# Performance work log

Hardware: AMD Instinct MI355X
Metric: run time of the kernel (lower is better)

## Reference

```python
import jax, jax.numpy as jnp
import numpy as np

N_NODES = 50000


def _gcn_conv(h, src, dst, W, b, n_nodes):
    """PyG GCNConv: add self-loops, symmetric deg^{-1/2} normalization,
    linear transform, scatter-add aggregation at target nodes."""
    h = h @ W  # [N, out]
    # self-loops
    loop = jnp.arange(n_nodes, dtype=src.dtype)
    s = jnp.concatenate([src, loop])  # source j
    d = jnp.concatenate([dst, loop])  # target i
    ones = jnp.ones(s.shape[0], dtype=h.dtype)
    deg = jax.ops.segment_sum(ones, d, num_segments=n_nodes)  # in-degree incl. self-loop
    dinv = jnp.where(deg > 0, jax.lax.rsqrt(deg), 0.0)
    norm = dinv[s] * dinv[d]  # [E+N]
    msg = h[s] * norm[:, None]  # gather + scale, [E+N, out]
    out = jax.ops.segment_sum(msg, d, num_segments=n_nodes)  # scatter-add
    return out + b


def reference(x, edge_index, q_emb, W1, b1, W2, b2, Wq, bq):
    src, dst = edge_index[0], edge_index[1]
    n = x.shape[0]
    # dropout rates are 0.0 -> identity
    h1 = jax.nn.relu(_gcn_conv(x, src, dst, W1, b1, n))
    h2 = _gcn_conv(h1, src, dst, W2, b2, n)
    ques = q_emb @ Wq + bq
    return (ques, h2)


def setup_inputs() -> dict:
    key = jax.random.key(0)
    ks = jax.random.split(key, 9)
    d = 128
    sc = 1.0 / np.sqrt(d)
    return {
        "x": jax.random.normal(ks[0], (N_NODES, d), dtype=jnp.float32),
        "edge_index": jax.random.randint(ks[1], (2, 800000), 0, N_NODES, dtype=jnp.int64),
        "q_emb": jax.random.normal(ks[2], (20000, d), dtype=jnp.float32),
        "W1": jax.random.normal(ks[3], (d, d), dtype=jnp.float32) * sc,
        "b1": jax.random.normal(ks[4], (d,), dtype=jnp.float32) * 0.01,
        "W2": jax.random.normal(ks[5], (d, d), dtype=jnp.float32) * sc,
        "b2": jax.random.normal(ks[6], (d,), dtype=jnp.float32) * 0.01,
        "Wq": jax.random.normal(ks[7], (d, d), dtype=jnp.float32) * sc,
        "bq": jax.random.normal(ks[8], (d,), dtype=jnp.float32) * 0.01,
    }
```

## Files before the change

### kernel.cpp

```cpp
#include <hip/hip_runtime.h>

#define D 128
#define NFB 256
#define CAP 64

typedef __attribute__((ext_vector_type(8))) short bf16x8;
typedef __attribute__((ext_vector_type(4))) float f32x4;

__device__ __forceinline__ unsigned short f2b(float v) {
    unsigned u = __float_as_uint(v);
    unsigned r = u + 0x7fffu + ((u >> 16) & 1u);
    return (unsigned short)(r >> 16);
}
__device__ __forceinline__ float b2f(unsigned short h) {
    return __uint_as_float(((unsigned)h) << 16);
}


__device__ __forceinline__ void gemm_body(const float* Af,
                                          const float* __restrict__ W,
                                          const float* bias, unsigned short* Cb,
                                          float* Cf, int M, int bid, int outf,
                                          char* smem) {
    int lane = threadIdx.x & 63;
    int wave = threadIdx.x >> 6;
    int m16 = (bid * 4 + wave) * 16;
    if (m16 >= M) return;
    int mrow = lane & 15;
    int quad = lane >> 4;

    f32x4 acc[8];
#pragma unroll
    for (int nt = 0; nt < 8; ++nt) acc[nt] = (f32x4){0.f, 0.f, 0.f, 0.f};

    int arow = m16 + mrow;

#pragma unroll
    for (int ks = 0; ks < 4; ++ks) {
        bf16x8 ah, al;
        const float* ap = Af + (size_t)arow * D + ks * 32 + quad * 8;
        float4 v0 = *(const float4*)ap;
        float4 v1 = *(const float4*)(ap + 4);
        float vv[8] = {v0.x, v0.y, v0.z, v0.w, v1.x, v1.y, v1.z, v1.w};
#pragma unroll
        for (int j = 0; j < 8; ++j) {
            unsigned short h = f2b(vv[j]);
            ah[j] = (short)h;
            al[j] = (short)f2b(vv[j] - b2f(h));
        }
#pragma unroll
        for (int nt = 0; nt < 8; ++nt) {
            const float* wp = W + (size_t)(ks * 32 + quad * 8) * D + nt * 16 + mrow;
            bf16x8 wf;
#pragma unroll
            for (int j = 0; j < 8; ++j) wf[j] = (short)f2b(wp[j * D]);
            acc[nt] = __builtin_amdgcn_mfma_f32_16x16x32_bf16(ah, wf, acc[nt], 0, 0, 0);
            acc[nt] = __builtin_amdgcn_mfma_f32_16x16x32_bf16(al, wf, acc[nt], 0, 0, 0);
        }
    }

    if (outf == 0) {
        unsigned short* myl = (unsigned short*)smem + wave * 16 * 136;
#pragma unroll
        for (int nt = 0; nt < 8; ++nt) {
            int col = nt * 16 + mrow;
#pragma unroll
            for (int r = 0; r < 4; ++r)
                myl[(quad * 4 + r) * 136 + col] = f2b(acc[nt][r]);
        }
#pragma unroll
        for (int R = 0; R < 16; ++R) {
            unsigned int v = *(const unsigned int*)&myl[R * 136 + lane * 2];
            ((unsigned int*)(Cb + (size_t)(m16 + R) * D))[lane] = v;
        }
    } else {
#pragma unroll
        for (int nt = 0; nt < 8; ++nt) {
            int col = nt * 16 + mrow;
            float bv = bias[col];
#pragma unroll
            for (int r = 0; r < 4; ++r)
                Cf[(size_t)(m16 + quad * 4 + r) * D + col] = acc[nt][r] + bv;
        }
    }
}

__global__ __launch_bounds__(256) void frontfill(const float* __restrict__ x,
                                                 const float* __restrict__ q,
                                                 const float* __restrict__ W1,
                                                 const float* __restrict__ Wq,
                                                 const float* __restrict__ bq,
                                                 unsigned short* __restrict__ Cb,
                                                 float* __restrict__ outq,
                                                 const int* __restrict__ src,
                                                 const int* __restrict__ dst,
                                                 int* __restrict__ cnt,
                                                 int* __restrict__ colv,
                                                 int N, int MQ, int E, int nbN) {
    __shared__ char smem[4 * 16 * 136 * 2];
    int b = blockIdx.x;
    if (b < NFB) {
        const int4* d4 = (const int4*)dst;
        const int4* s4 = (const int4*)src;
        int n4 = E >> 2;
        int stride = NFB * 256;
        for (int idx = b * 256 + threadIdx.x; idx < n4; idx += stride) {
            int4 dv = d4[idx];
            int4 sv = s4[idx];
            int slot;
            slot = atomicAdd(&cnt[dv.x], 1);
            if (slot < CAP) colv[(size_t)dv.x * CAP + slot] = sv.x;
            slot = atomicAdd(&cnt[dv.y], 1);
            if (slot < CAP) colv[(size_t)dv.y * CAP + slot] = sv.y;
            slot = atomicAdd(&cnt[dv.z], 1);
            if (slot < CAP) colv[(size_t)dv.z * CAP + slot] = sv.z;
            slot = atomicAdd(&cnt[dv.w], 1);
            if (slot < CAP) colv[(size_t)dv.w * CAP + slot] = sv.w;
        }
        for (int e = (n4 << 2) + b * 256 + threadIdx.x; e < E; e += stride) {
            int d = dst[e];
            int slot = atomicAdd(&cnt[d], 1);
            if (slot < CAP) colv[(size_t)d * CAP + slot] = src[e];
        }
        return;
    }
    b -= NFB;
    if (b < nbN)
        gemm_body(x, W1, nullptr, Cb, nullptr, N, b, 0, smem);
    else
        gemm_body(q, Wq, bq, nullptr, outq, MQ, b - nbN, 1, smem);
}

__device__ __forceinline__ void agg_node(const bf16x8* __restrict__ T8,
                                         const int* __restrict__ colv,
                                         const int* __restrict__ cnt,
                                         int i, int ci, int lane, int g, int l16,
                                         float acc[8]) {
#pragma unroll
    for (int k = 0; k < 8; ++k) acc[k] = 0.f;
    int jv = 0;
    float wv = 0.f;
    if (lane < ci) {
        jv = colv[i * CAP + lane];
        wv = rsqrtf((float)(cnt[jv] + 1));
    }
    int t = 0;
    for (; t + 16 <= ci; t += 16) {
        int j0 = __shfl(jv, t + g);
        int j1 = __shfl(jv, t + 4 + g);
        int j2 = __shfl(jv, t + 8 + g);
        int j3 = __shfl(jv, t + 12 + g);
        float w0 = __shfl(wv, t + g);
        float w1 = __shfl(wv, t + 4 + g);
        float w2 = __shfl(wv, t + 8 + g);
        float w3 = __shfl(wv, t + 12 + g);
        bf16x8 r0 = T8[(size_t)j0 * 16 + l16];
        bf16x8 r1 = T8[(size_t)j1 * 16 + l16];
        bf16x8 r2 = T8[(size_t)j2 * 16 + l16];
        bf16x8 r3 = T8[(size_t)j3 * 16 + l16];
#pragma unroll
        for (int k = 0; k < 8; ++k) acc[k] = fmaf(w0, b2f((unsigned short)r0[k]), acc[k]);
#pragma unroll
        for (int k = 0; k < 8; ++k) acc[k] = fmaf(w1, b2f((unsigned short)r1[k]), acc[k]);
#pragma unroll
        for (int k = 0; k < 8; ++k) acc[k] = fmaf(w2, b2f((unsigned short)r2[k]), acc[k]);
#pragma unroll
        for (int k = 0; k < 8; ++k) acc[k] = fmaf(w3, b2f((unsigned short)r3[k]), acc[k]);
    }
    for (; t < ci; t += 4) {
        int j = __shfl(jv, t + g);
        float w = __shfl(wv, t + g);
        if (w > 0.f) {
            bf16x8 r = T8[(size_t)j * 16 + l16];
#pragma unroll
            for (int k = 0; k < 8; ++k) acc[k] = fmaf(w, b2f((unsigned short)r[k]), acc[k]);
        }
    }
#pragma unroll
    for (int k = 0; k < 8; ++k) {
        acc[k] += __shfl_xor(acc[k], 16);
        acc[k] += __shfl_xor(acc[k], 32);
    }
}

__global__ __launch_bounds__(512) void agg1_gemm(const unsigned short* __restrict__ Tb,
                                                 const int* __restrict__ colv,
                                                 const int* __restrict__ cnt,
                                                 const float* __restrict__ bias,
                                                 const float* __restrict__ W2,
                                                 unsigned short* __restrict__ Cb2,
                                                 int N) {
    __shared__ unsigned short AH[16 * 136];
    __shared__ unsigned short AL[16 * 136];
    int wave = threadIdx.x >> 6;
    int lane = threadIdx.x & 63;
    int g = lane >> 4;
    int l16 = lane & 15;
    int node0 = blockIdx.x * 16;
    const bf16x8* T8 = (const bf16x8*)Tb;

#pragma unroll
    for (int sub = 0; sub < 2; ++sub) {
        int row = wave * 2 + sub;
        int i = node0 + row;
        float acc[8];
        if (i < N) {
            int deg = cnt[i];
            int ci = (deg < CAP) ? deg : CAP;
            agg_node(T8, colv, cnt, i, ci, lane, g, l16, acc);
            if (g == 0) {
                float di = rsqrtf((float)(deg + 1));
                bf16x8 selfr = T8[(size_t)i * 16 + l16];
                float4 b0 = ((const float4*)bias)[l16 * 2];
                float4 b1v = ((const float4*)bias)[l16 * 2 + 1];
                float bb[8] = {b0.x, b0.y, b0.z, b0.w, b1v.x, b1v.y, b1v.z, b1v.w};
                bf16x8 h, l;
#pragma unroll
                for (int k = 0; k < 8; ++k) {
                    float r = di * acc[k] + di * di * b2f((unsigned short)selfr[k]) + bb[k];
                    r = fmaxf(r, 0.f);
                    unsigned short hh = f2b(r);
                    h[k] = (short)hh;
                    l[k] = (short)f2b(r - b2f(hh));
                }
                *(bf16x8*)&AH[row * 136 + l16 * 8] = h;
                *(bf16x8*)&AL[row * 136 + l16 * 8] = l;
            }
        } else if (g == 0) {
            bf16x8 z = (bf16x8){0, 0, 0, 0, 0, 0, 0, 0};
            *(bf16x8*)&AH[row * 136 + l16 * 8] = z;
            *(bf16x8*)&AL[row * 136 + l16 * 8] = z;
        }
    }
    __syncthreads();

    int nt = wave;
    int mrow = l16;
    int quad = g;
    f32x4 acc2 = (f32x4){0.f, 0.f, 0.f, 0.f};
#pragma unroll
    for (int ks = 0; ks < 4; ++ks) {
        bf16x8 ah = *(const bf16x8*)&AH[mrow * 136 + ks * 32 + quad * 8];
        bf16x8 al = *(const bf16x8*)&AL[mrow * 136 + ks * 32 + quad * 8];
        const float* wp = W2 + (size_t)(ks * 32 + quad * 8) * D + nt * 16 + mrow;
        bf16x8 wf;
#pragma unroll
        for (int j = 0; j < 8; ++j) wf[j] = (short)f2b(wp[j * D]);
        acc2 = __builtin_amdgcn_mfma_f32_16x16x32_bf16(ah, wf, acc2, 0, 0, 0);
        acc2 = __builtin_amdgcn_mfma_f32_16x16x32_bf16(al, wf, acc2, 0, 0, 0);
    }
    __syncthreads();
    {
        int col = nt * 16 + mrow;
#pragma unroll
        for (int r = 0; r < 4; ++r) {
            int gi = node0 + quad * 4 + r;
            float dr = (gi < N) ? rsqrtf((float)(cnt[gi] + 1)) : 0.f;
            AH[(quad * 4 + r) * 136 + col] = f2b(acc2[r] * dr);
        }
    }
    __syncthreads();
#pragma unroll
    for (int k = 0; k < 2; ++k) {
        int idx = threadIdx.x + k * 512;
        int row = idx >> 6;
        int c = idx & 63;
        if (node0 + row < N) {
            unsigned int v = *(const unsigned int*)&AH[row * 136 + c * 2];
            ((unsigned int*)(Cb2 + (size_t)(node0 + row) * D))[c] = v;
        }
    }
}

__global__ __launch_bounds__(512) void aggregate2(const unsigned short* __restrict__ Tb,
                                                  const int* __restrict__ colv,
                                                  const int* __restrict__ cnt,
                                                  const float* __restrict__ bias,
                                                  float* __restrict__ Of, int N) {
    int wave = threadIdx.x >> 6;
    int lane = threadIdx.x & 63;
    int i = blockIdx.x * 8 + wave;
    if (i >= N) return;
    int g = lane >> 4;
    int l16 = lane & 15;
    const bf16x8* T8 = (const bf16x8*)Tb;

    int deg = cnt[i];
    int ci = (deg < CAP) ? deg : CAP;
    bf16x8 selfr = T8[(size_t)i * 16 + l16];
    float4 b0 = ((const float4*)bias)[l16 * 2];
    float4 b1v = ((const float4*)bias)[l16 * 2 + 1];

    float acc[8];
#pragma unroll
    for (int k = 0; k < 8; ++k) acc[k] = 0.f;

    int jv = (lane < ci) ? colv[i * CAP + lane] : 0;
    int t = 0;
    for (; t + 16 <= ci; t += 16) {
        int j0 = __shfl(jv, t + g);
        int j1 = __shfl(jv, t + 4 + g);
        int j2 = __shfl(jv, t + 8 + g);
        int j3 = __shfl(jv, t + 12 + g);
        bf16x8 r0 = T8[(size_t)j0 * 16 + l16];
        bf16x8 r1 = T8[(size_t)j1 * 16 + l16];
        bf16x8 r2 = T8[(size_t)j2 * 16 + l16];
        bf16x8 r3 = T8[(size_t)j3 * 16 + l16];
#pragma unroll
        for (int k = 0; k < 8; ++k)
            acc[k] += b2f((unsigned short)r0[k]) + b2f((unsigned short)r1[k]) +
                      b2f((unsigned short)r2[k]) + b2f((unsigned short)r3[k]);
    }
    for (; t < ci; t += 4) {
        int j = __shfl(jv, t + g);
        if (t + g < ci) {
            bf16x8 r = T8[(size_t)j * 16 + l16];
#pragma unroll
            for (int k = 0; k < 8; ++k) acc[k] += b2f((unsigned short)r[k]);
        }
    }

#pragma unroll
    for (int k = 0; k < 8; ++k) {
        acc[k] += __shfl_xor(acc[k], 16);
        acc[k] += __shfl_xor(acc[k], 32);
    }

    if (g == 0) {
        float di = rsqrtf((float)(deg + 1));
        float bb[8] = {b0.x, b0.y, b0.z, b0.w, b1v.x, b1v.y, b1v.z, b1v.w};
        float4 r0, r1;
        r0.x = di * (acc[0] + b2f((unsigned short)selfr[0])) + bb[0];
        r0.y = di * (acc[1] + b2f((unsigned short)selfr[1])) + bb[1];
        r0.z = di * (acc[2] + b2f((unsigned short)selfr[2])) + bb[2];
        r0.w = di * (acc[3] + b2f((unsigned short)selfr[3])) + bb[3];
        r1.x = di * (acc[4] + b2f((unsigned short)selfr[4])) + bb[4];
        r1.y = di * (acc[5] + b2f((unsigned short)selfr[5])) + bb[5];
        r1.z = di * (acc[6] + b2f((unsigned short)selfr[6])) + bb[6];
        r1.w = di * (acc[7] + b2f((unsigned short)selfr[7])) + bb[7];
        ((float4*)Of)[(size_t)i * 32 + l16 * 2] = r0;
        ((float4*)Of)[(size_t)i * 32 + l16 * 2 + 1] = r1;
    }
}


static inline char* carve(char*& w, size_t bytes) {
    char* p = w;
    w += (bytes + 255) & ~(size_t)255;
    return p;
}

extern "C" void kernel_launch(void* const* d_in, const int* in_sizes, int n_in,
                              void* d_out, int out_size, void* d_ws, size_t ws_size,
                              hipStream_t stream) {
    const float* x  = (const float*)d_in[0];
    const int*   ei = (const int*)d_in[1];
    const float* q  = (const float*)d_in[2];
    const float* W1 = (const float*)d_in[3];
    const float* b1 = (const float*)d_in[4];
    const float* W2 = (const float*)d_in[5];
    const float* b2 = (const float*)d_in[6];
    const float* Wq = (const float*)d_in[7];
    const float* bq = (const float*)d_in[8];

    int N  = in_sizes[0] / D;
    int E  = in_sizes[1] / 2;
    int MQ = in_sizes[2] / D;

    const int* srcv = ei;
    const int* dstv = ei + E;

    char* w = (char*)d_ws;
    unsigned short* Cb   = (unsigned short*)carve(w, (size_t)N * D * 2);
    unsigned short* Cb2  = (unsigned short*)carve(w, (size_t)N * D * 2);
    int*            colv = (int*)carve(w, (size_t)N * CAP * 4);
    int*            cnt  = (int*)carve(w, (size_t)N * 4);

    float* outq = (float*)d_out;
    float* outh = outq + (size_t)MQ * D;

    int nbN = (N + 63) / 64;
    int nbQ = (MQ + 63) / 64;

    hipMemsetAsync(cnt, 0, (size_t)N * 4, stream);
    frontfill<<<NFB + nbN + nbQ, 256, 0, stream>>>(x, q, W1, Wq, bq, Cb, outq,
                                                   srcv, dstv, cnt, colv,
                                                   N, MQ, E, nbN);
    agg1_gemm<<<(N + 15) / 16, 512, 0, stream>>>(Cb, colv, cnt, b1, W2, Cb2, N);
    aggregate2<<<(N + 7) / 8, 512, 0, stream>>>(Cb2, colv, cnt, b2, outh, N);
}
```

Baseline: 227.4 us.

## Fuse all stages into one persistent cooperative kernel with grid syncs

Replaces the memset plus three kernel launches with a single cooperative persistent kernel that zeroes counts, builds adjacency and runs the GEMMs, then does both aggregations, separated by grid-wide syncs. Each block covers multiple virtual tiles in grid-stride loops. The aim is to remove launch gaps and kernel-boundary drain/tail costs. It adds grid-sync overhead, can lower occupancy because shared memory is larger and registers are shared across phases, and falls back to the old path if the cooperative launch fails.

```diff
diff --git a/kernel.cpp b/kernel.cpp
--- a/kernel.cpp
+++ b/kernel.cpp
@@ -1,4 +1,7 @@
 #include <hip/hip_runtime.h>
+#include <hip/hip_cooperative_groups.h>
+
+namespace cg = cooperative_groups;
 
 #define D 128
 #define NFB 256
@@ -17,13 +20,42 @@
 }
 
 
-__device__ __forceinline__ void gemm_body(const float* Af,
+__device__ __forceinline__ void fill_vb(int vb, int ltid,
+                                        const int* __restrict__ src,
+                                        const int* __restrict__ dst,
+                                        int* __restrict__ cnt,
+                                        int* __restrict__ colv, int E) {
+    const int4* d4 = (const int4*)dst;
+    const int4* s4 = (const int4*)src;
+    int n4 = E >> 2;
+    int stride = NFB * 256;
+    for (int idx = vb * 256 + ltid; idx < n4; idx += stride) {
+        int4 dv = d4[idx];
+        int4 sv = s4[idx];
+        int slot;
+        slot = atomicAdd(&cnt[dv.x], 1);
+        if (slot < CAP) colv[(size_t)dv.x * CAP + slot] = sv.x;
+        slot = atomicAdd(&cnt[dv.y], 1);
+        if (slot < CAP) colv[(size_t)dv.y * CAP + slot] = sv.y;
+        slot = atomicAdd(&cnt[dv.z], 1);
+        if (slot < CAP) colv[(size_t)dv.z * CAP + slot] = sv.z;
+        slot = atomicAdd(&cnt[dv.w], 1);
+        if (slot < CAP) colv[(size_t)dv.w * CAP + slot] = sv.w;
+    }
+    for (int e = (n4 << 2) + vb * 256 + ltid; e < E; e += stride) {
+        int d = dst[e];
+        int slot = atomicAdd(&cnt[d], 1);
+        if (slot < CAP) colv[(size_t)d * CAP + slot] = src[e];
+    }
+}
+
+__device__ __forceinline__ void gemm_tile(const float* Af,
                                           const float* __restrict__ W,
                                           const float* bias, unsigned short* Cb,
                                           float* Cf, int M, int bid, int outf,
-                                          char* smem) {
-    int lane = threadIdx.x & 63;
-    int wave = threadIdx.x >> 6;
+                                          char* smem, int ltid) {
+    int lane = ltid & 63;
+    int wave = ltid >> 6;
     int m16 = (bid * 4 + wave) * 16;
     if (m16 >= M) return;
     int mrow = lane & 15;
@@ -84,6 +116,279 @@
         }
     }
 }
+
+__device__ __forceinline__ void agg_node(const bf16x8* __restrict__ T8,
+                                         const int* __restrict__ colv,
+                                         const int* __restrict__ cnt,
+                                         int i, int ci, int lane, int g, int l16,
+                                         float acc[8]) {
+#pragma unroll
+    for (int k = 0; k < 8; ++k) acc[k] = 0.f;
+    int jv = 0;
+    float wv = 0.f;
+    if (lane < ci) {
+        jv = colv[i * CAP + lane];
+        wv = rsqrtf((float)(cnt[jv] + 1));
+    }
+    int t = 0;
+    for (; t + 16 <= ci; t += 16) {
+        int j0 = __shfl(jv, t + g);
+        int j1 = __shfl(jv, t + 4 + g);
+        int j2 = __shfl(jv, t + 8 + g);
+        int j3 = __shfl(jv, t + 12 + g);
+        float w0 = __shfl(wv, t + g);
+        float w1 = __shfl(wv, t + 4 + g);
+        float w2 = __shfl(wv, t + 8 + g);
+        float w3 = __shfl(wv, t + 12 + g);
+        bf16x8 r0 = T8[(size_t)j0 * 16 + l16];
+        bf16x8 r1 = T8[(size_t)j1 * 16 + l16];
+        bf16x8 r2 = T8[(size_t)j2 * 16 + l16];
+        bf16x8 r3 = T8[(size_t)j3 * 16 + l16];
+#pragma unroll
+        for (int k = 0; k < 8; ++k) acc[k] = fmaf(w0, b2f((unsigned short)r0[k]), acc[k]);
+#pragma unroll
+        for (int k = 0; k < 8; ++k) acc[k] = fmaf(w1, b2f((unsigned short)r1[k]), acc[k]);
+#pragma unroll
+        for (int k = 0; k < 8; ++k) acc[k] = fmaf(w2, b2f((unsigned short)r2[k]), acc[k]);
+#pragma unroll
+        for (int k = 0; k < 8; ++k) acc[k] = fmaf(w3, b2f((unsigned short)r3[k]), acc[k]);
+    }
+    for (; t < ci; t += 4) {
+        int j = __shfl(jv, t + g);
+        float w = __shfl(wv, t + g);
+        if (w > 0.f) {
+            bf16x8 r = T8[(size_t)j * 16 + l16];
+#pragma unroll
+            for (int k = 0; k < 8; ++k) acc[k] = fmaf(w, b2f((unsigned short)r[k]), acc[k]);
+        }
+    }
+#pragma unroll
+    for (int k = 0; k < 8; ++k) {
+        acc[k] += __shfl_xor(acc[k], 16);
+        acc[k] += __shfl_xor(acc[k], 32);
+    }
+}
+
+__device__ __forceinline__ void agg1_body(int grp, unsigned short* AH,
+                                          unsigned short* AL,
+                                          const unsigned short* __restrict__ Tb,
+                                          const int* __restrict__ colv,
+                                          const int* __restrict__ cnt,
+                                          const float* __restrict__ bias,
+                                          const float* __restrict__ W2,
+                                          unsigned short* __restrict__ Cb2, int N) {
+    __syncthreads();
+    int wave = threadIdx.x >> 6;
+    int lane = threadIdx.x & 63;
+    int g = lane >> 4;
+    int l16 = lane & 15;
+    int node0 = grp * 16;
+    const bf16x8* T8 = (const bf16x8*)Tb;
+
+#pragma unroll
+    for (int sub = 0; sub < 2; ++sub) {
+        int row = wave * 2 + sub;
+        int i = node0 + row;
+        float acc[8];
+        if (i < N) {
+            int deg = cnt[i];
+            int ci = (deg < CAP) ? deg : CAP;
+            agg_node(T8, colv, cnt, i, ci, lane, g, l16, acc);
+            if (g == 0) {
+                float di = rsqrtf((float)(deg + 1));
+                bf16x8 selfr = T8[(size_t)i * 16 + l16];
+                float4 b0 = ((const float4*)bias)[l16 * 2];
+                float4 b1v = ((const float4*)bias)[l16 * 2 + 1];
+                float bb[8] = {b0.x, b0.y, b0.z, b0.w, b1v.x, b1v.y, b1v.z, b1v.w};
+                bf16x8 h, l;
+#pragma unroll
+                for (int k = 0; k < 8; ++k) {
+                    float r = di * acc[k] + di * di * b2f((unsigned short)selfr[k]) + bb[k];
+                    r = fmaxf(r, 0.f);
+                    unsigned short hh = f2b(r);
+                    h[k] = (short)hh;
+                    l[k] = (short)f2b(r - b2f(hh));
+                }
+                *(bf16x8*)&AH[row * 136 + l16 * 8] = h;
+                *(bf16x8*)&AL[row * 136 + l16 * 8] = l;
+            }
+        } else if (g == 0) {
+            bf16x8 z = (bf16x8){0, 0, 0, 0, 0, 0, 0, 0};
+            *(bf16x8*)&AH[row * 136 + l16 * 8] = z;
+            *(bf16x8*)&AL[row * 136 + l16 * 8] = z;
+        }
+    }
+    __syncthreads();
+
+    int nt = wave;
+    int mrow = l16;
+    int quad = g;
+    f32x4 acc2 = (f32x4){0.f, 0.f, 0.f, 0.f};
+#pragma unroll
+    for (int ks = 0; ks < 4; ++ks) {
+        bf16x8 ah = *(const bf16x8*)&AH[mrow * 136 + ks * 32 + quad * 8];
+        bf16x8 al = *(const bf16x8*)&AL[mrow * 136 + ks * 32 + quad * 8];
+        const float* wp = W2 + (size_t)(ks * 32 + quad * 8) * D + nt * 16 + mrow;
+        bf16x8 wf;
+#pragma unroll
+        for (int j = 0; j < 8; ++j) wf[j] = (short)f2b(wp[j * D]);
+        acc2 = __builtin_amdgcn_mfma_f32_16x16x32_bf16(ah, wf, acc2, 0, 0, 0);
+        acc2 = __builtin_amdgcn_mfma_f32_16x16x32_bf16(al, wf, acc2, 0, 0, 0);
+    }
+    __syncthreads();
+    {
+        int col = nt * 16 + mrow;
+#pragma unroll
+        for (int r = 0; r < 4; ++r) {
+            int gi = node0 + quad * 4 + r;
+            float dr = (gi < N) ? rsqrtf((float)(cnt[gi] + 1)) : 0.f;
+            AH[(quad * 4 + r) * 136 + col] = f2b(acc2[r] * dr);
+        }
+    }
+    __syncthreads();
+#pragma unroll
+    for (int k = 0; k < 2; ++k) {
+        int idx = threadIdx.x + k * 512;
+        int row = idx >> 6;
+        int c = idx & 63;
+        if (node0 + row < N) {
+            unsigned int v = *(const unsigned int*)&AH[row * 136 + c * 2];
+            ((unsigned int*)(Cb2 + (size_t)(node0 + row) * D))[c] = v;
+        }
+    }
+}
+
+__device__ __forceinline__ void agg2_body(int grp,
+                                          const unsigned short* __restrict__ Tb,
+                                          const int* __restrict__ colv,
+                                          const int* __restrict__ cnt,
+                                          const float* __restrict__ bias,
+                                          float* __restrict__ Of, int N) {
+    int wave = threadIdx.x >> 6;
+    int lane = threadIdx.x & 63;
+    int i = grp * 8 + wave;
+    if (i >= N) return;
+    int g = lane >> 4;
+    int l16 = lane & 15;
+    const bf16x8* T8 = (const bf16x8*)Tb;
+
+    int deg = cnt[i];
+    int ci = (deg < CAP) ? deg : CAP;
+    bf16x8 selfr = T8[(size_t)i * 16 + l16];
+    float4 b0 = ((const float4*)bias)[l16 * 2];
+    float4 b1v = ((const float4*)bias)[l16 * 2 + 1];
+
+    float acc[8];
+#pragma unroll
+    for (int k = 0; k < 8; ++k) acc[k] = 0.f;
+
+    int jv = (lane < ci) ? colv[i * CAP + lane] : 0;
+    int t = 0;
+    for (; t + 16 <= ci; t += 16) {
+        int j0 = __shfl(jv, t + g);
+        int j1 = __shfl(jv, t + 4 + g);
+        int j2 = __shfl(jv, t + 8 + g);
+        int j3 = __shfl(jv, t + 12 + g);
+        bf16x8 r0 = T8[(size_t)j0 * 16 + l16];
+        bf16x8 r1 = T8[(size_t)j1 * 16 + l16];
+        bf16x8 r2 = T8[(size_t)j2 * 16 + l16];
+        bf16x8 r3 = T8[(size_t)j3 * 16 + l16];
+#pragma unroll
+        for (int k = 0; k < 8; ++k)
+            acc[k] += b2f((unsigned short)r0[k]) + b2f((unsigned short)r1[k]) +
+                      b2f((unsigned short)r2[k]) + b2f((unsigned short)r3[k]);
+    }
+    for (; t < ci; t += 4) {
+        int j = __shfl(jv, t + g);
+        if (t + g < ci) {
+            bf16x8 r = T8[(size_t)j * 16 + l16];
+#pragma unroll
+            for (int k = 0; k < 8; ++k) acc[k] += b2f((unsigned short)r[k]);
+        }
+    }
+
+#pragma unroll
+    for (int k = 0; k < 8; ++k) {
+        acc[k] += __shfl_xor(acc[k], 16);
+        acc[k] += __shfl_xor(acc[k], 32);
+    }
+
+    if (g == 0) {
+        float di = rsqrtf((float)(deg + 1));
+        float bb[8] = {b0.x, b0.y, b0.z, b0.w, b1v.x, b1v.y, b1v.z, b1v.w};
+        float4 r0, r1;
+        r0.x = di * (acc[0] + b2f((unsigned short)selfr[0])) + bb[0];
+        r0.y = di * (acc[1] + b2f((unsigned short)selfr[1])) + bb[1];
+        r0.z = di * (acc[2] + b2f((unsigned short)selfr[2])) + bb[2];
+        r0.w = di * (acc[3] + b2f((unsigned short)selfr[3])) + bb[3];
+        r1.x = di * (acc[4] + b2f((unsigned short)selfr[4])) + bb[4];
+        r1.y = di * (acc[5] + b2f((unsigned short)selfr[5])) + bb[5];
+        r1.z = di * (acc[6] + b2f((unsigned short)selfr[6])) + bb[6];
+        r1.w = di * (acc[7] + b2f((unsigned short)selfr[7])) + bb[7];
+        ((float4*)Of)[(size_t)i * 32 + l16 * 2] = r0;
+        ((float4*)Of)[(size_t)i * 32 + l16 * 2 + 1] = r1;
+    }
+}
+
+
+__global__ __launch_bounds__(512) void mega(const float* x, const float* q,
+                                            const float* W1, const float* Wq,
+                                            const float* bq, const float* W2,
+                                            const float* b1, const float* b2,
+                                            unsigned short* Cb, unsigned short* Cb2,
+                                            float* outq, float* outh,
+                                            const int* src, const int* dst,
+                                            int* cnt, int* colv,
+                                            int N, int MQ, int E, int nbN, int nbQ) {
+    __shared__ char smem[2 * 4 * 16 * 136 * 2];
+    cg::grid_group grid = cg::this_grid();
+    int G = gridDim.x;
+
+    {
+        int n4 = N >> 2;
+        for (int idx = blockIdx.x * 512 + threadIdx.x; idx < n4; idx += G * 512)
+            ((int4*)cnt)[idx] = make_int4(0, 0, 0, 0);
+        for (int k = (n4 << 2) + blockIdx.x * 512 + threadIdx.x; k < N; k += G * 512)
+            cnt[k] = 0;
+    }
+    grid.sync();
+
+    {
+        int half = threadIdx.x >> 8;
+        int ltid = threadIdx.x & 255;
+        int nvb = NFB + nbN + nbQ;
+        for (int vb = blockIdx.x * 2 + half; vb < nvb; vb += G * 2) {
+            if (vb < NFB) {
+                fill_vb(vb, ltid, src, dst, cnt, colv, E);
+            } else {
+                int b = vb - NFB;
+                if (b < nbN)
+                    gemm_tile(x, W1, nullptr, Cb, nullptr, N, b, 0,
+                              smem + half * 17408, ltid);
+                else
+                    gemm_tile(q, Wq, bq, nullptr, outq, MQ, b - nbN, 1,
+                              smem + half * 17408, ltid);
+            }
+        }
+    }
+    grid.sync();
+
+    {
+        unsigned short* AH = (unsigned short*)smem;
+        unsigned short* AL = (unsigned short*)(smem + 4352);
+        int ngrp = (N + 15) / 16;
+        for (int grp = blockIdx.x; grp < ngrp; grp += G)
+            agg1_body(grp, AH, AL, Cb, colv, cnt, b1, W2, Cb2, N);
+    }
+    grid.sync();
+
+    {
+        int ngrp = (N + 7) / 8;
+        for (int grp = blockIdx.x; grp < ngrp; grp += G)
+            agg2_body(grp, Cb2, colv, cnt, b2, outh, N);
+    }
+}
+
 
 __global__ __launch_bounds__(256) void frontfill(const float* __restrict__ x,
                                                  const float* __restrict__ q,
@@ -100,87 +405,14 @@
     __shared__ char smem[4 * 16 * 136 * 2];
     int b = blockIdx.x;
     if (b < NFB) {
-        const int4* d4 = (const int4*)dst;
-        const int4* s4 = (const int4*)src;
-        int n4 = E >> 2;
-        int stride = NFB * 256;
-        for (int idx = b * 256 + threadIdx.x; idx < n4; idx += stride) {
-            int4 dv = d4[idx];
-            int4 sv = s4[idx];
-            int slot;
-            slot = atomicAdd(&cnt[dv.x], 1);
-            if (slot < CAP) colv[(size_t)dv.x * CAP + slot] = sv.x;
-            slot = atomicAdd(&cnt[dv.y], 1);
-            if (slot < CAP) colv[(size_t)dv.y * CAP + slot] = sv.y;
-            slot = atomicAdd(&cnt[dv.z], 1);
-            if (slot < CAP) colv[(size_t)dv.z * CAP + slot] = sv.z;
-            slot = atomicAdd(&cnt[dv.w], 1);
-            if (slot < CAP) colv[(size_t)dv.w * CAP + slot] = sv.w;
-        }
-        for (int e = (n4 << 2) + b * 256 + threadIdx.x; e < E; e += stride) {
-            int d = dst[e];
-            int slot = atomicAdd(&cnt[d], 1);
-            if (slot < CAP) colv[(size_t)d * CAP + slot] = src[e];
-        }
+        fill_vb(b, threadIdx.x, src, dst, cnt, colv, E);
         return;
     }
     b -= NFB;
     if (b < nbN)
-        gemm_body(x, W1, nullptr, Cb, nullptr, N, b, 0, smem);
+        gemm_tile(x, W1, nullptr, Cb, nullptr, N, b, 0, smem, threadIdx.x);
     else
-        gemm_body(q, Wq, bq, nullptr, outq, MQ, b - nbN, 1, smem);
-}
-
-__device__ __forceinline__ void agg_node(const bf16x8* __restrict__ T8,
-                                         const int* __restrict__ colv,
-                                         const int* __restrict__ cnt,
-                                         int i, int ci, int lane, int g, int l16,
-                                         float acc[8]) {
-#pragma unroll
-    for (int k = 0; k < 8; ++k) acc[k] = 0.f;
-    int jv = 0;
-    float wv = 0.f;
-    if (lane < ci) {
-        jv = colv[i * CAP + lane];
-        wv = rsqrtf((float)(cnt[jv] + 1));
-    }
-    int t = 0;
-    for (; t + 16 <= ci; t += 16) {
-        int j0 = __shfl(jv, t + g);
-        int j1 = __shfl(jv, t + 4 + g);
-        int j2 = __shfl(jv, t + 8 + g);
-        int j3 = __shfl(jv, t + 12 + g);
-        float w0 = __shfl(wv, t + g);
-        float w1 = __shfl(wv, t + 4 + g);
-        float w2 = __shfl(wv, t + 8 + g);
-        float w3 = __shfl(wv, t + 12 + g);
-        bf16x8 r0 = T8[(size_t)j0 * 16 + l16];
-        bf16x8 r1 = T8[(size_t)j1 * 16 + l16];
-        bf16x8 r2 = T8[(size_t)j2 * 16 + l16];
-        bf16x8 r3 = T8[(size_t)j3 * 16 + l16];
-#pragma unroll
-        for (int k = 0; k < 8; ++k) acc[k] = fmaf(w0, b2f((unsigned short)r0[k]), acc[k]);
-#pragma unroll
-        for (int k = 0; k < 8; ++k) acc[k] = fmaf(w1, b2f((unsigned short)r1[k]), acc[k]);
-#pragma unroll
-        for (int k = 0; k < 8; ++k) acc[k] = fmaf(w2, b2f((unsigned short)r2[k]), acc[k]);
-#pragma unroll
-        for (int k = 0; k < 8; ++k) acc[k] = fmaf(w3, b2f((unsigned short)r3[k]), acc[k]);
-    }
-    for (; t < ci; t += 4) {
-        int j = __shfl(jv, t + g);
-        float w = __shfl(wv, t + g);
-        if (w > 0.f) {
-            bf16x8 r = T8[(size_t)j * 16 + l16];
-#pragma unroll
-            for (int k = 0; k < 8; ++k) acc[k] = fmaf(w, b2f((unsigned short)r[k]), acc[k]);
-        }
-    }
-#pragma unroll
-    for (int k = 0; k < 8; ++k) {
-        acc[k] += __shfl_xor(acc[k], 16);
-        acc[k] += __shfl_xor(acc[k], 32);
-    }
+        gemm_tile(q, Wq, bq, nullptr, outq, MQ, b - nbN, 1, smem, threadIdx.x);
 }
 
 __global__ __launch_bounds__(512) void agg1_gemm(const unsigned short* __restrict__ Tb,
@@ -192,84 +424,7 @@
                                                  int N) {
     __shared__ unsigned short AH[16 * 136];
     __shared__ unsigned short AL[16 * 136];
-    int wave = threadIdx.x >> 6;
-    int lane = threadIdx.x & 63;
-    int g = lane >> 4;
-    int l16 = lane & 15;
-    int node0 = blockIdx.x * 16;
-    const bf16x8* T8 = (const bf16x8*)Tb;
-
-#pragma unroll
-    for (int sub = 0; sub < 2; ++sub) {
-        int row = wave * 2 + sub;
-        int i = node0 + row;
-        float acc[8];
-        if (i < N) {
-            int deg = cnt[i];
-            int ci = (deg < CAP) ? deg : CAP;
-            agg_node(T8, colv, cnt, i, ci, lane, g, l16, acc);
-            if (g == 0) {
-                float di = rsqrtf((float)(deg + 1));
-                bf16x8 selfr = T8[(size_t)i * 16 + l16];
-                float4 b0 = ((const float4*)bias)[l16 * 2];
-                float4 b1v = ((const float4*)bias)[l16 * 2 + 1];
-                float bb[8] = {b0.x, b0.y, b0.z, b0.w, b1v.x, b1v.y, b1v.z, b1v.w};
-                bf16x8 h, l;
-#pragma unroll
-                for (int k = 0; k < 8; ++k) {
-                    float r = di * acc[k] + di * di * b2f((unsigned short)selfr[k]) + bb[k];
-                    r = fmaxf(r, 0.f);
-                    unsigned short hh = f2b(r);
-                    h[k] = (short)hh;
-                    l[k] = (short)f2b(r - b2f(hh));
-                }
-                *(bf16x8*)&AH[row * 136 + l16 * 8] = h;
-                *(bf16x8*)&AL[row * 136 + l16 * 8] = l;
-            }
-        } else if (g == 0) {
-            bf16x8 z = (bf16x8){0, 0, 0, 0, 0, 0, 0, 0};
-            *(bf16x8*)&AH[row * 136 + l16 * 8] = z;
-            *(bf16x8*)&AL[row * 136 + l16 * 8] = z;
-        }
-    }
-    __syncthreads();
-
-    int nt = wave;
-    int mrow = l16;
-    int quad = g;
-    f32x4 acc2 = (f32x4){0.f, 0.f, 0.f, 0.f};
-#pragma unroll
-    for (int ks = 0; ks < 4; ++ks) {
-        bf16x8 ah = *(const bf16x8*)&AH[mrow * 136 + ks * 32 + quad * 8];
-        bf16x8 al = *(const bf16x8*)&AL[mrow * 136 + ks * 32 + quad * 8];
-        const float* wp = W2 + (size_t)(ks * 32 + quad * 8) * D + nt * 16 + mrow;
-        bf16x8 wf;
-#pragma unroll
-        for (int j = 0; j < 8; ++j) wf[j] = (short)f2b(wp[j * D]);
-        acc2 = __builtin_amdgcn_mfma_f32_16x16x32_bf16(ah, wf, acc2, 0, 0, 0);
-        acc2 = __builtin_amdgcn_mfma_f32_16x16x32_bf16(al, wf, acc2, 0, 0, 0);
-    }
-    __syncthreads();
-    {
-        int col = nt * 16 + mrow;
-#pragma unroll
-        for (int r = 0; r < 4; ++r) {
-            int gi = node0 + quad * 4 + r;
-            float dr = (gi < N) ? rsqrtf((float)(cnt[gi] + 1)) : 0.f;
-            AH[(quad * 4 + r) * 136 + col] = f2b(acc2[r] * dr);
-        }
-    }
-    __syncthreads();
-#pragma unroll
-    for (int k = 0; k < 2; ++k) {
-        int idx = threadIdx.x + k * 512;
-        int row = idx >> 6;
-        int c = idx & 63;
-        if (node0 + row < N) {
-            unsigned int v = *(const unsigned int*)&AH[row * 136 + c * 2];
-            ((unsigned int*)(Cb2 + (size_t)(node0 + row) * D))[c] = v;
-        }
-    }
+    agg1_body(blockIdx.x, AH, AL, Tb, colv, cnt, bias, W2, Cb2, N);
 }
 
 __global__ __launch_bounds__(512) void aggregate2(const unsigned short* __restrict__ Tb,
@@ -277,70 +432,7 @@
                                                   const int* __restrict__ cnt,
                                                   const float* __restrict__ bias,
                                                   float* __restrict__ Of, int N) {
-    int wave = threadIdx.x >> 6;
-    int lane = threadIdx.x & 63;
-    int i = blockIdx.x * 8 + wave;
-    if (i >= N) return;
-    int g = lane >> 4;
-    int l16 = lane & 15;
-    const bf16x8* T8 = (const bf16x8*)Tb;
-
-    int deg = cnt[i];
-    int ci = (deg < CAP) ? deg : CAP;
-    bf16x8 selfr = T8[(size_t)i * 16 + l16];
-    float4 b0 = ((const float4*)bias)[l16 * 2];
-    float4 b1v = ((const float4*)bias)[l16 * 2 + 1];
-
-    float acc[8];
-#pragma unroll
-    for (int k = 0; k < 8; ++k) acc[k] = 0.f;
-
-    int jv = (lane < ci) ? colv[i * CAP + lane] : 0;
-    int t = 0;
-    for (; t + 16 <= ci; t += 16) {
-        int j0 = __shfl(jv, t + g);
-        int j1 = __shfl(jv, t + 4 + g);
-        int j2 = __shfl(jv, t + 8 + g);
-        int j3 = __shfl(jv, t + 12 + g);
-        bf16x8 r0 = T8[(size_t)j0 * 16 + l16];
-        bf16x8 r1 = T8[(size_t)j1 * 16 + l16];
-        bf16x8 r2 = T8[(size_t)j2 * 16 + l16];
-        bf16x8 r3 = T8[(size_t)j3 * 16 + l16];
-#pragma unroll
-        for (int k = 0; k < 8; ++k)
-            acc[k] += b2f((unsigned short)r0[k]) + b2f((unsigned short)r1[k]) +
-                      b2f((unsigned short)r2[k]) + b2f((unsigned short)r3[k]);
-    }
-    for (; t < ci; t += 4) {
-        int j = __shfl(jv, t + g);
-        if (t + g < ci) {
-            bf16x8 r = T8[(size_t)j * 16 + l16];
-#pragma unroll
-            for (int k = 0; k < 8; ++k) acc[k] += b2f((unsigned short)r[k]);
-        }
-    }
-
-#pragma unroll
-    for (int k = 0; k < 8; ++k) {
-        acc[k] += __shfl_xor(acc[k], 16);
-        acc[k] += __shfl_xor(acc[k], 32);
-    }
-
-    if (g == 0) {
-        float di = rsqrtf((float)(deg + 1));
-        float bb[8] = {b0.x, b0.y, b0.z, b0.w, b1v.x, b1v.y, b1v.z, b1v.w};
-        float4 r0, r1;
-        r0.x = di * (acc[0] + b2f((unsigned short)selfr[0])) + bb[0];
-        r0.y = di * (acc[1] + b2f((unsigned short)selfr[1])) + bb[1];
-        r0.z = di * (acc[2] + b2f((unsigned short)selfr[2])) + bb[2];
-        r0.w = di * (acc[3] + b2f((unsigned short)selfr[3])) + bb[3];
-        r1.x = di * (acc[4] + b2f((unsigned short)selfr[4])) + bb[4];
-        r1.y = di * (acc[5] + b2f((unsigned short)selfr[5])) + bb[5];
-        r1.z = di * (acc[6] + b2f((unsigned short)selfr[6])) + bb[6];
-        r1.w = di * (acc[7] + b2f((unsigned short)selfr[7])) + bb[7];
-        ((float4*)Of)[(size_t)i * 32 + l16 * 2] = r0;
-        ((float4*)Of)[(size_t)i * 32 + l16 * 2 + 1] = r1;
-    }
+    agg2_body(blockIdx.x, Tb, colv, cnt, bias, Of, N);
 }
 
 
@@ -382,10 +474,45 @@
     int nbN = (N + 63) / 64;
     int nbQ = (MQ + 63) / 64;
 
-    hipMemsetAsync(cnt, 0, (size_t)N * 4, stream);
-    frontfill<<<NFB + nbN + nbQ, 256, 0, stream>>>(x, q, W1, Wq, bq, Cb, outq,
-                                                   srcv, dstv, cnt, colv,
-                                                   N, MQ, E, nbN);
-    agg1_gemm<<<(N + 15) / 16, 512, 0, stream>>>(Cb, colv, cnt, b1, W2, Cb2, N);
-    aggregate2<<<(N + 7) / 8, 512, 0, stream>>>(Cb2, colv, cnt, b2, outh, N);
-}
+    static int maxBlocks = -2;
+    if (maxBlocks == -2) {
+        int dev = 0, numCU = 0, perCU = 0;
+        if (hipGetDevice(&dev) == hipSuccess &&
+            hipDeviceGetAttribute(&numCU, hipDeviceAttributeMultiprocessorCount,
+                                  dev) == hipSuccess &&
+            hipOccupancyMaxActiveBlocksPerMultiprocessor(&perCU, mega, 512, 0) ==
+                hipSuccess &&
+            perCU > 0 && numCU > 0)
+            maxBlocks = perCU * numCU;
+        else
+            maxBlocks = -1;
+    }
+
+    bool launched = false;
+    if (maxBlocks > 0) {
+        int G = maxBlocks > 2048 ? 2048 : maxBlocks;
+        void* args[] = {(void*)&x,   (void*)&q,    (void*)&W1,   (void*)&Wq,
+                        (void*)&bq,  (void*)&W2,   (void*)&b1,   (void*)&b2,
+                        (void*)&Cb,  (void*)&Cb2,  (void*)&outq, (void*)&outh,
+                        (void*)&srcv,(void*)&dstv, (void*)&cnt,  (void*)&colv,
+                        (void*)&N,   (void*)&MQ,   (void*)&E,    (void*)&nbN,
+                        (void*)&nbQ};
+        hipError_t err = hipLaunchCooperativeKernel((const void*)mega, dim3(G),
+                                                    dim3(512), args, 0, stream);
+        if (err == hipSuccess) {
+            launched = true;
+        } else {
+            (void)hipGetLastError();
+            maxBlocks = -1;
+        }
+    }
+
+    if (!launched) {
+        hipMemsetAsync(cnt, 0, (size_t)N * 4, stream);
+        frontfill<<<NFB + nbN + nbQ, 256, 0, stream>>>(x, q, W1, Wq, bq, Cb, outq,
+                                                       srcv, dstv, cnt, colv,
+                                                       N, MQ, E, nbN);
+        agg1_gemm<<<(N + 15) / 16, 512, 0, stream>>>(Cb, colv, cnt, b1, W2, Cb2, N);
+        aggregate2<<<(N + 7) / 8, 512, 0, stream>>>(Cb2, colv, cnt, b2, outh, N);
+    }
+}
```

After: 229.1 us. No clear change (+0.7%).
